# Optimization experiments

Hardware: AMD Instinct MI355X
Metric: run time of the kernel (lower is better)

Reference implementation:

```python
import jax, jax.numpy as jnp
import numpy as np

N = 20000        # nodes
E = 160000       # directed edges (before self loops)
NODE_DIM = 1287
HEADS = 4
C1, C2, C3 = 128, 256, 128
ACT_SLOPE = 0.15   # module's LeakyReLU between layers
GAT_SLOPE = 0.2    # PyG GATConv default negative_slope


def _gat_layer(x, src, dst, W, att_src, att_dst, bias, heads, out_dim, concat):
    # x: [N, in] ; W: [in, heads*out] ; att_*: [heads, out] ; bias: [heads*out] or [out]
    h = (x @ W).reshape(N, heads, out_dim)                      # [N, H, C]
    a_s = jnp.einsum('nhc,hc->nh', h, att_src)                  # [N, H]
    a_d = jnp.einsum('nhc,hc->nh', h, att_dst)                  # [N, H]
    e = jax.nn.leaky_relu(a_s[src] + a_d[dst], GAT_SLOPE)       # [Etot, H]
    # segment softmax over incoming edges of each dst node (self loops => no empty segments)
    m = jax.ops.segment_max(e, dst, num_segments=N)             # [N, H]
    w = jnp.exp(e - m[dst])
    den = jax.ops.segment_sum(w, dst, num_segments=N)           # [N, H]
    alpha = w / den[dst]                                        # [Etot, H]
    msg = h[src] * alpha[:, :, None]                            # [Etot, H, C]
    out = jax.ops.segment_sum(msg, dst, num_segments=N)         # [N, H, C]
    out = out.reshape(N, heads * out_dim) if concat else out.mean(axis=1)
    return out + bias


def setup_inputs() -> dict:
    key = jax.random.key(0)
    ks = jax.random.split(key, 22)
    s = 0.05
    x = jax.random.normal(ks[0], (N, NODE_DIM), jnp.float32)
    edge_index = jax.random.randint(ks[1], (2, E), 0, N, dtype=jnp.int64)
    inp = {
        'x': x, 'edge_index': edge_index,
        'W1': jax.random.normal(ks[2], (NODE_DIM, HEADS * C1), jnp.float32) * s,
        'as1': jax.random.normal(ks[3], (HEADS, C1), jnp.float32) * s,
        'ad1': jax.random.normal(ks[4], (HEADS, C1), jnp.float32) * s,
        'b1': jnp.zeros((HEADS * C1,), jnp.float32),
        'W2': jax.random.normal(ks[5], (HEADS * C1, HEADS * C2), jnp.float32) * s,
        'as2': jax.random.normal(ks[6], (HEADS, C2), jnp.float32) * s,
        'ad2': jax.random.normal(ks[7], (HEADS, C2), jnp.float32) * s,
        'b2': jnp.zeros((HEADS * C2,), jnp.float32),
        # conv3: 1024 -> 128, 1 head, no concat
        'W3': jax.random.normal(ks[8], (HEADS * C2, C3), jnp.float32) * s,
        'as3': jax.random.normal(ks[9], (1, C3), jnp.float32) * s,
        'ad3': jax.random.normal(ks[10], (1, C3), jnp.float32) * s,
        'b3': jnp.zeros((C3,), jnp.float32),
        # pre_fc: 128 -> 16
        'pw': jax.random.normal(ks[11], (C3, 16), jnp.float32) * s,
        'pb': jnp.zeros((16,), jnp.float32),
        # fc fallback: Linear(16,32) -> LeakyReLU(0.15) -> Linear(32,2)
        'f1w': jax.random.normal(ks[12], (16, 32), jnp.float32) * s,
        'f1b': jnp.zeros((32,), jnp.float32),
        'f2w': jax.random.normal(ks[13], (32, 2), jnp.float32) * s,
        'f2b': jnp.zeros((2,), jnp.float32),
    }
    return inp


def reference(x, edge_index, W1, as1, ad1, b1, W2, as2, ad2, b2,
              W3, as3, ad3, b3, pw, pb, f1w, f1b, f2w, f2b):
    loop = jnp.arange(N, dtype=edge_index.dtype)
    src = jnp.concatenate([edge_index[0], loop])   # PyG add_self_loops=True
    dst = jnp.concatenate([edge_index[1], loop])
    h = _gat_layer(x, src, dst, W1, as1, ad1, b1, HEADS, C1, True)
    h = jax.nn.leaky_relu(h, ACT_SLOPE)            # dropout = identity (eval)
    h = _gat_layer(h, src, dst, W2, as2, ad2, b2, HEADS, C2, True)
    h = jax.nn.leaky_relu(h, ACT_SLOPE)
    h = _gat_layer(h, src, dst, W3, as3, ad3, b3, 1, C3, False)
    h = jax.nn.leaky_relu(h, ACT_SLOPE)
    h = h @ pw + pb                                 # pre_fc (128 -> 16)
    h = jax.nn.leaky_relu(h @ f1w + f1b, ACT_SLOPE)
    return h @ f2w + f2b                            # [N, 2] logits
```

## Files before the change

kernel.cpp:

```cpp
#include <hip/hip_runtime.h>
#include <hip/hip_bf16.h>
#include <cstdint>
#include <cstddef>

#define LRELU(x, s) ((x) > 0.f ? (x) : (s) * (x))

typedef __attribute__((ext_vector_type(8))) short bf16x8;
typedef __attribute__((ext_vector_type(4))) float f32x4;

__device__ __forceinline__ float bflo(uint v) { return __uint_as_float(v << 16); }
__device__ __forceinline__ float bfhi(uint v) { return __uint_as_float(v & 0xffff0000u); }
__device__ __forceinline__ ushort f2bf(float f) {
  const uint u = __float_as_uint(f);
  return (ushort)((u + 0x7fffu + ((u >> 16) & 1u)) >> 16);
}

__device__ __forceinline__ void async16(const ushort* g, ushort* l) {
  __builtin_amdgcn_global_load_lds(
      (const __attribute__((address_space(1))) unsigned int*)g,
      (__attribute__((address_space(3))) unsigned int*)l, 16, 0, 0);
}

#define WAITCNT_VM(n) (0xF70 | (n))

__global__ void cast_pad_rows(const float* __restrict__ in, ushort* __restrict__ out,
                              int rows, int K, int Kp) {
  const int P4 = Kp >> 2;
  const long long idx = (long long)blockIdx.x * blockDim.x + threadIdx.x;
  if (idx >= (long long)rows * P4) return;
  const int r = (int)(idx / P4);
  const int c = ((int)(idx - (long long)r * P4)) << 2;
  const float* p = in + (size_t)r * K + c;
  float v0 = 0.f, v1 = 0.f, v2 = 0.f, v3 = 0.f;
  if (c + 3 < K) { v0 = p[0]; v1 = p[1]; v2 = p[2]; v3 = p[3]; }
  else {
    if (c + 0 < K) v0 = p[0];
    if (c + 1 < K) v1 = p[1];
    if (c + 2 < K) v2 = p[2];
    if (c + 3 < K) v3 = p[3];
  }
  uint2 o;
  o.x = (uint)f2bf(v0) | ((uint)f2bf(v1) << 16);
  o.y = (uint)f2bf(v2) | ((uint)f2bf(v3) << 16);
  *(uint2*)(out + (size_t)r * Kp + c) = o;
}

__global__ void cast_W_T(const float* __restrict__ W, ushort* __restrict__ Wt,
                         int K, int Nn, int Kp) {
  __shared__ float tile[32][33];
  const int kt = blockIdx.x * 32;
  const int nt = blockIdx.y * 32;
  const int tx = threadIdx.x;
  const int ty = threadIdx.y;
  for (int r = ty; r < 32; r += 8) {
    const int k = kt + r, nn = nt + tx;
    tile[r][tx] = (k < K && nn < Nn) ? W[(size_t)k * Nn + nn] : 0.f;
  }
  __syncthreads();
  for (int r = ty; r < 32; r += 8) {
    const int nn = nt + r, k = kt + tx;
    if (nn < Nn && k < Kp) Wt[(size_t)nn * Kp + k] = f2bf(tile[tx][r]);
  }
}

template <int TM>
__global__ __launch_bounds__(256) void gemm_bf16(
    const ushort* __restrict__ A, const ushort* __restrict__ Bt, ushort* __restrict__ C,
    int M, int N, int Kp,
    const float* __restrict__ AS, const float* __restrict__ AD,
    float* __restrict__ asb, float* __restrict__ adb, int H, int headC) {
  constexpr int MI = TM / 32;
  constexpr int LPG = (TM == 128) ? 4 : 3;
  __shared__ ushort sA[2 * TM * 32];
  __shared__ ushort sB[2 * 128 * 32];
  const int tid = threadIdx.x;
  const int wave = tid >> 6;
  const int lane = tid & 63;
  const int tilesN = N >> 7;
  const int bx = blockIdx.x % tilesN;
  const int by = blockIdx.x / tilesN;
  const int wrow = (wave >> 1) * (TM / 2);
  const int wcol = (wave & 1) * 64;
  const int quad = lane >> 4;
  const int ml = lane & 15;

  const int seg = (lane & 3) * 8;
  const int rB0 = wave * 32 + (lane >> 2);
  const int gB0 = bx * 128 + rB0;
  const ushort* pB0 = Bt + (size_t)gB0 * Kp + seg;
  const ushort* pB1 = Bt + (size_t)(gB0 + 16) * Kp + seg;
  ushort* lB0 = &sB[(wave * 32) * 32];
  ushort* lB1 = &sB[(wave * 32 + 16) * 32];
  const ushort *pA0, *pA1;
  ushort *lA0, *lA1;
  if constexpr (TM == 128) {
    const int r0 = wave * 32 + (lane >> 2);
    pA0 = A + (size_t)min(by * TM + r0, M - 1) * Kp + seg;
    pA1 = A + (size_t)min(by * TM + r0 + 16, M - 1) * Kp + seg;
    lA0 = &sA[(wave * 32) * 32];
    lA1 = &sA[(wave * 32 + 16) * 32];
  } else {
    const int r0 = wave * 16 + (lane >> 2);
    pA0 = A + (size_t)min(by * TM + r0, M - 1) * Kp + seg;
    pA1 = nullptr;
    lA0 = &sA[(wave * 16) * 32];
    lA1 = nullptr;
  }

  const int nIter = Kp >> 5;
  auto issue = [&](int it, int p) {
    const int k0 = it << 5;
    const int oa = p * TM * 32;
    const int ob_ = p * 128 * 32;
    async16(pA0 + k0, lA0 + oa);
    if constexpr (TM == 128) async16(pA1 + k0, lA1 + oa);
    async16(pB0 + k0, lB0 + ob_);
    async16(pB1 + k0, lB1 + ob_);
  };

  f32x4 acc[MI][4];
#pragma unroll
  for (int mi = 0; mi < MI; mi++)
#pragma unroll
    for (int ni = 0; ni < 4; ni++)
#pragma unroll
      for (int e = 0; e < 4; e++) acc[mi][ni][e] = 0.f;

  issue(0, 0);
  if (nIter > 1) issue(1, 1);
  int p = 0;
  for (int it = 0; it < nIter; ++it) {
    if (it + 1 < nIter) __builtin_amdgcn_s_waitcnt(WAITCNT_VM(LPG));
    else __builtin_amdgcn_s_waitcnt(WAITCNT_VM(0));
    __builtin_amdgcn_s_barrier();
    const ushort* bA = &sA[p * TM * 32];
    const ushort* bB = &sB[p * 128 * 32];
    bf16x8 af[MI], bfr[4];
#pragma unroll
    for (int mi = 0; mi < MI; mi++)
      af[mi] = *(const bf16x8*)&bA[(wrow + mi * 16 + ml) * 32 + quad * 8];
#pragma unroll
    for (int ni = 0; ni < 4; ni++)
      bfr[ni] = *(const bf16x8*)&bB[(wcol + ni * 16 + ml) * 32 + quad * 8];
#pragma unroll
    for (int mi = 0; mi < MI; mi++)
#pragma unroll
      for (int ni = 0; ni < 4; ni++)
        acc[mi][ni] = __builtin_amdgcn_mfma_f32_16x16x32_bf16(af[mi], bfr[ni], acc[mi][ni], 0, 0, 0);
    if (it + 2 < nIter) {
      __builtin_amdgcn_s_barrier();
      issue(it + 2, p);
    }
    p ^= 1;
  }

#pragma unroll
  for (int mi = 0; mi < MI; mi++) {
#pragma unroll
    for (int r = 0; r < 4; r++) {
      const int row = by * TM + wrow + mi * 16 + quad * 4 + r;
      if (row < M) {
#pragma unroll
        for (int ni = 0; ni < 4; ni++) {
          const int col = bx * 128 + wcol + ni * 16 + ml;
          C[(size_t)row * N + col] = f2bf(acc[mi][ni][r]);
        }
      }
    }
  }

  if (asb != nullptr) {
    float asv[4], adv[4];
#pragma unroll
    for (int ni = 0; ni < 4; ni++) {
      const int col = bx * 128 + wcol + ni * 16 + ml;
      asv[ni] = AS[col];
      adv[ni] = AD[col];
    }
    const int hh = (bx * 128 + wcol) / headC;
#pragma unroll
    for (int mi = 0; mi < MI; mi++) {
#pragma unroll
      for (int r = 0; r < 4; r++) {
        float ps = acc[mi][0][r] * asv[0] + acc[mi][1][r] * asv[1] +
                   acc[mi][2][r] * asv[2] + acc[mi][3][r] * asv[3];
        float pd = acc[mi][0][r] * adv[0] + acc[mi][1][r] * adv[1] +
                   acc[mi][2][r] * adv[2] + acc[mi][3][r] * adv[3];
#pragma unroll
        for (int off = 1; off < 16; off <<= 1) {
          ps += __shfl_xor(ps, off);
          pd += __shfl_xor(pd, off);
        }
        if (ml == 0) {
          const int row = by * TM + wrow + mi * 16 + quad * 4 + r;
          if (row < M) {
            atomicAdd(&asb[row * H + hh], ps);
            atomicAdd(&adb[row * H + hh], pd);
          }
        }
      }
    }
  }
}

__global__ void count_deg(const int* __restrict__ dst, int E, int* __restrict__ deg) {
  const int t = blockIdx.x * blockDim.x + threadIdx.x;
  if (t < E) atomicAdd(&deg[dst[t]], 1);
}

__global__ __launch_bounds__(1024) void scan_kernel(const int* __restrict__ deg,
                                                    int* __restrict__ rowptr,
                                                    int* __restrict__ cursor, int n) {
  __shared__ int swsum[16];
  __shared__ int carry_s;
  const int t = threadIdx.x;
  const int wv = t >> 6, lane = t & 63;
  if (t == 0) carry_s = 0;
  __syncthreads();
  for (int base = 0; base < n; base += 1024) {
    const int i = base + t;
    const int v = (i < n) ? (deg[i] + 1) : 0;
    int sc = v;
#pragma unroll
    for (int off = 1; off < 64; off <<= 1) {
      const int u = __shfl_up(sc, off);
      if (lane >= off) sc += u;
    }
    if (lane == 63) swsum[wv] = sc;
    __syncthreads();
    if (t < 16) {
      int x = swsum[t];
#pragma unroll
      for (int off = 1; off < 16; off <<= 1) {
        const int u = __shfl_up(x, off);
        if (t >= off) x += u;
      }
      swsum[t] = x;
    }
    __syncthreads();
    const int incl = sc + (wv == 0 ? 0 : swsum[wv - 1]) + carry_s;
    if (i < n) { rowptr[i + 1] = incl; cursor[i] = incl - v; }
    if (base == 0 && t == 0) rowptr[0] = 0;
    __syncthreads();
    if (t == 0) carry_s += swsum[15];
    __syncthreads();
  }
}

__global__ void scatter_edges(const int* __restrict__ esrc, const int* __restrict__ edst,
                              int E, int Etot, int* __restrict__ cursor,
                              int* __restrict__ csr_src) {
  const int t = blockIdx.x * blockDim.x + threadIdx.x;
  if (t >= Etot) return;
  int s, d;
  if (t < E) { s = esrc[t]; d = edst[t]; } else { s = t - E; d = s; }
  const int pos = atomicAdd(&cursor[d], 1);
  csr_src[pos] = s;
}

template <int H, int C>
__global__ __launch_bounds__(256) void gat_agg_wave(
    const ushort* __restrict__ hb, const int* __restrict__ rowptr,
    const int* __restrict__ csr_src, const float* __restrict__ a_s,
    const float* __restrict__ a_d, const float* __restrict__ bias,
    ushort* __restrict__ outb, float act_slope, int Nn) {
  constexpr int HC = H * C;
  constexpr int NU = HC / 2;
  constexpr int PPT = NU / 128;
  const int n = blockIdx.x * 4 + (threadIdx.x >> 6);
  const int lane = threadIdx.x & 63;
  if (n >= Nn) return;
  float ad_n[H];
#pragma unroll
  for (int h = 0; h < H; h++) ad_n[h] = a_d[n * H + h];
  const int start = rowptr[n], end = rowptr[n + 1];
  f32x4 acc[PPT];
#pragma unroll
  for (int q = 0; q < PPT; q++)
#pragma unroll
    for (int e = 0; e < 4; e++) acc[q][e] = 0.f;
  float den[H];
#pragma unroll
  for (int h = 0; h < H; h++) den[h] = 0.f;

  for (int base = start; base < end; base += 64) {
    const int cnt = min(64, end - base);
    int s = 0;
    float w[H];
#pragma unroll
    for (int h = 0; h < H; h++) w[h] = 0.f;
    if (lane < cnt) {
      s = csr_src[base + lane];
      float asv[H];
      if constexpr (H == 4) {
        const float4 t4 = *(const float4*)(a_s + s * 4);
        asv[0] = t4.x; asv[1] = t4.y; asv[2] = t4.z; asv[3] = t4.w;
      } else {
        asv[0] = a_s[s];
      }
#pragma unroll
      for (int h = 0; h < H; h++) {
        float lg = asv[h] + ad_n[h];
        lg = LRELU(lg, 0.2f);
        w[h] = __expf(lg);
        den[h] += w[h];
      }
    }
    for (int j = 0; j < cnt; j++) {
      const int sj = __shfl(s, j);
      float wj[H];
#pragma unroll
      for (int h = 0; h < H; h++) wj[h] = __shfl(w[h], j);
      const uint2* hp = (const uint2*)(hb + (size_t)sj * HC);
#pragma unroll
      for (int q = 0; q < PPT; q++) {
        const int pu = q * 128 + lane * 2;
        const uint2 v = hp[q * 64 + lane];
        const float wq = wj[(2 * pu) / C];
        acc[q][0] += wq * bflo(v.x);
        acc[q][1] += wq * bfhi(v.x);
        acc[q][2] += wq * bflo(v.y);
        acc[q][3] += wq * bfhi(v.y);
      }
    }
  }
#pragma unroll
  for (int h = 0; h < H; h++) {
#pragma unroll
    for (int off = 1; off < 64; off <<= 1) den[h] += __shfl_xor(den[h], off);
    den[h] = 1.f / den[h];
  }
#pragma unroll
  for (int q = 0; q < PPT; q++) {
    const int pu = q * 128 + lane * 2;
    const float iv = den[(2 * pu) / C];
    const float4 b4 = *(const float4*)(bias + 2 * pu);
    const float o0 = LRELU(acc[q][0] * iv + b4.x, act_slope);
    const float o1 = LRELU(acc[q][1] * iv + b4.y, act_slope);
    const float o2 = LRELU(acc[q][2] * iv + b4.z, act_slope);
    const float o3 = LRELU(acc[q][3] * iv + b4.w, act_slope);
    uint2 o;
    o.x = (uint)f2bf(o0) | ((uint)f2bf(o1) << 16);
    o.y = (uint)f2bf(o2) | ((uint)f2bf(o3) << 16);
    ((uint2*)outb)[(size_t)n * (NU / 2) + q * 64 + lane] = o;
  }
}

__global__ __launch_bounds__(64) void gat_agg3_mlp(
    const ushort* __restrict__ hb, const int* __restrict__ rowptr,
    const int* __restrict__ csr_src, const float* __restrict__ a_s,
    const float* __restrict__ a_d, const float* __restrict__ b3,
    const float* __restrict__ pw, const float* __restrict__ pb,
    const float* __restrict__ f1w, const float* __restrict__ f1b,
    const float* __restrict__ f2w, const float* __restrict__ f2b,
    float* __restrict__ out) {
  const int n = blockIdx.x;
  const int tid = threadIdx.x;
  __shared__ float sx[128];
  __shared__ float s1[16];
  __shared__ float s2[32];
  const float ad_n = a_d[n];
  const int start = rowptr[n], end = rowptr[n + 1];
  float2 acc = make_float2(0.f, 0.f);
  float den = 0.f;
  for (int base = start; base < end; base += 64) {
    const int cnt = min(64, end - base);
    int s = 0;
    float w = 0.f;
    if (tid < cnt) {
      s = csr_src[base + tid];
      float lg = a_s[s] + ad_n;
      lg = LRELU(lg, 0.2f);
      w = __expf(lg);
      den += w;
    }
    for (int j = 0; j < cnt; j++) {
      const int sj = __shfl(s, j);
      const float wj = __shfl(w, j);
      const uint v = ((const uint*)(hb + (size_t)sj * 128))[tid];
      acc.x += wj * bflo(v);
      acc.y += wj * bfhi(v);
    }
  }
#pragma unroll
  for (int off = 1; off < 64; off <<= 1) den += __shfl_xor(den, off);
  const float iv = 1.f / den;
  sx[2 * tid]     = LRELU(acc.x * iv + b3[2 * tid], 0.15f);
  sx[2 * tid + 1] = LRELU(acc.y * iv + b3[2 * tid + 1], 0.15f);
  __syncthreads();
  if (tid < 16) {
    float a = pb[tid];
    for (int c = 0; c < 128; c++) a += sx[c] * pw[c * 16 + tid];
    s1[tid] = a;
  }
  __syncthreads();
  if (tid < 32) {
    float a = f1b[tid];
    for (int c = 0; c < 16; c++) a += s1[c] * f1w[c * 32 + tid];
    s2[tid] = LRELU(a, 0.15f);
  }
  __syncthreads();
  if (tid < 2) {
    float a = f2b[tid];
    for (int c = 0; c < 32; c++) a += s2[c] * f2w[c * 2 + tid];
    out[(size_t)n * 2 + tid] = a;
  }
}

extern "C" void kernel_launch(void* const* d_in, const int* in_sizes, int n_in,
                              void* d_out, int out_size, void* d_ws, size_t ws_size,
                              hipStream_t stream) {
  const float* x   = (const float*)d_in[0];
  const int* ei    = (const int*)d_in[1];
  const float* W1  = (const float*)d_in[2];
  const float* as1 = (const float*)d_in[3];
  const float* ad1 = (const float*)d_in[4];
  const float* b1  = (const float*)d_in[5];
  const float* W2  = (const float*)d_in[6];
  const float* as2 = (const float*)d_in[7];
  const float* ad2 = (const float*)d_in[8];
  const float* b2  = (const float*)d_in[9];
  const float* W3  = (const float*)d_in[10];
  const float* as3 = (const float*)d_in[11];
  const float* ad3 = (const float*)d_in[12];
  const float* b3  = (const float*)d_in[13];
  const float* pw  = (const float*)d_in[14];
  const float* pb  = (const float*)d_in[15];
  const float* f1w = (const float*)d_in[16];
  const float* f1b = (const float*)d_in[17];
  const float* f2w = (const float*)d_in[18];
  const float* f2b = (const float*)d_in[19];
  float* out = (float*)d_out;

  const int N = in_sizes[0] / 1287;
  const int E = in_sizes[1] / 2;
  const int Etot = E + N;
  const int* esrc = ei;
  const int* edst = ei + E;
  const int K1 = 1287, K1p = 1312;

  char* ws = (char*)d_ws;
  size_t off = 0;
  auto alloc = [&](size_t bytes) -> void* {
    void* p = ws + off;
    off = (off + bytes + 255) & ~(size_t)255;
    return p;
  };
  ushort* hb  = (ushort*)alloc((size_t)N * 1024 * 2);
  ushort* ob  = (ushort*)alloc((size_t)N * 1024 * 2);
  ushort* xb  = (ushort*)alloc((size_t)N * K1p * 2);
  ushort* W1t = (ushort*)alloc((size_t)512 * K1p * 2);
  ushort* W2t = (ushort*)alloc((size_t)1024 * 512 * 2);
  ushort* W3t = (ushort*)alloc((size_t)128 * 1024 * 2);
  float* av   = (float*)alloc((size_t)N * 8 * sizeof(float));
  int* deg    = (int*)alloc((size_t)N * sizeof(int));
  int* rowptr = (int*)alloc((size_t)(N + 1) * sizeof(int));
  int* cursor = (int*)alloc((size_t)N * sizeof(int));
  int* csr    = (int*)alloc((size_t)Etot * sizeof(int));
  float* asb = av;
  float* adb = av + (size_t)N * 4;

  hipMemsetAsync(deg, 0, (size_t)N * sizeof(int), stream);
  count_deg<<<(E + 255) / 256, 256, 0, stream>>>(edst, E, deg);
  scan_kernel<<<1, 1024, 0, stream>>>(deg, rowptr, cursor, N);
  scatter_edges<<<(Etot + 255) / 256, 256, 0, stream>>>(esrc, edst, E, Etot, cursor, csr);

  {
    const long long nx = (long long)N * (K1p / 4);
    cast_pad_rows<<<(int)((nx + 255) / 256), 256, 0, stream>>>(x, xb, N, K1, K1p);
    cast_W_T<<<dim3(K1p / 32, (512 + 31) / 32), dim3(32, 8), 0, stream>>>(W1, W1t, K1, 512, K1p);
    cast_W_T<<<dim3(512 / 32, 1024 / 32), dim3(32, 8), 0, stream>>>(W2, W2t, 512, 1024, 512);
    cast_W_T<<<dim3(1024 / 32, 128 / 32), dim3(32, 8), 0, stream>>>(W3, W3t, 1024, 128, 1024);
  }

  const int tilesM = (N + 127) / 128;
  const int tilesM64 = (N + 63) / 64;
  const int aggBlocks = (N + 3) / 4;

  {
    const int H = 4, C = 128, HC = 512;
    hipMemsetAsync(av, 0, (size_t)N * 8 * sizeof(float), stream);
    gemm_bf16<128><<<tilesM * (HC / 128), 256, 0, stream>>>(xb, W1t, hb, N, HC, K1p,
                                                            as1, ad1, asb, adb, H, C);
    gat_agg_wave<4, 128><<<aggBlocks, 256, 0, stream>>>(hb, rowptr, csr, asb, adb,
                                                        b1, ob, 0.15f, N);
  }
  {
    const int H = 4, C = 256, HC = 1024;
    hipMemsetAsync(av, 0, (size_t)N * 8 * sizeof(float), stream);
    gemm_bf16<128><<<tilesM * (HC / 128), 256, 0, stream>>>(ob, W2t, hb, N, HC, 512,
                                                            as2, ad2, asb, adb, H, C);
    gat_agg_wave<4, 256><<<aggBlocks, 256, 0, stream>>>(hb, rowptr, csr, asb, adb,
                                                        b2, ob, 0.15f, N);
  }
  {
    const int HC = 128;
    hipMemsetAsync(av, 0, (size_t)N * 8 * sizeof(float), stream);
    gemm_bf16<64><<<tilesM64 * (HC / 128), 256, 0, stream>>>(ob, W3t, hb, N, HC, 1024,
                                                             as3, ad3, asb, adb, 1, 128);
    gat_agg3_mlp<<<N, 64, 0, stream>>>(hb, rowptr, csr, asb, adb, b3,
                                       pw, pb, f1w, f1b, f2w, f2b, out);
  }
}
```

Measured before the change: 525.6 us.

## Reorder layer-2 GAT to aggregate before projecting, fold attention into precomputed vectors

Layer 2 now computes attention logits directly from the 512-wide input using precomputed W2·att vectors. It then aggregates the 512-wide input features per head before the GEMM, with the GEMM reading head-specific slices of the aggregated buffer and applying bias plus LeakyReLU in its epilogue. This shrinks gather traffic from 1024-wide to 512-wide rows per edge, at the cost of writing a 2048-wide aggregated buffer. The GEMM also moves to a triple-buffered LDS pipeline that issues loads right after the barrier, dropping the second barrier, and uses M-major block ordering.

Result: slower. 549.3 us (+4.5%).

```diff
diff --git a/kernel.cpp b/kernel.cpp
--- a/kernel.cpp
+++ b/kernel.cpp
@@ -63,45 +63,61 @@
   }
 }
 
+__global__ void make_v2(const float* __restrict__ W2, const float* __restrict__ as2,
+                        const float* __restrict__ ad2, float* __restrict__ v) {
+  const int t = blockIdx.x * blockDim.x + threadIdx.x;
+  if (t >= 4096) return;
+  const int k = t >> 3, j = t & 7;
+  const int h = j & 3;
+  const float* att = (j >= 4) ? ad2 : as2;
+  const float* wrow = W2 + (size_t)k * 1024 + h * 256;
+  const float* ap = att + h * 256;
+  float a = 0.f;
+  for (int c = 0; c < 256; c++) a += wrow[c] * ap[c];
+  v[k * 8 + j] = a;
+}
+
 template <int TM>
 __global__ __launch_bounds__(256) void gemm_bf16(
     const ushort* __restrict__ A, const ushort* __restrict__ Bt, ushort* __restrict__ C,
-    int M, int N, int Kp,
+    int M, int N, int Kp, int Ars, int AheadStride, int headColsA,
+    const float* __restrict__ bias, float slope,
     const float* __restrict__ AS, const float* __restrict__ AD,
     float* __restrict__ asb, float* __restrict__ adb, int H, int headC) {
   constexpr int MI = TM / 32;
   constexpr int LPG = (TM == 128) ? 4 : 3;
-  __shared__ ushort sA[2 * TM * 32];
-  __shared__ ushort sB[2 * 128 * 32];
+  __shared__ ushort sA[3 * TM * 32];
+  __shared__ ushort sB[3 * 128 * 32];
   const int tid = threadIdx.x;
   const int wave = tid >> 6;
   const int lane = tid & 63;
-  const int tilesN = N >> 7;
-  const int bx = blockIdx.x % tilesN;
-  const int by = blockIdx.x / tilesN;
+  const int tilesM = (M + TM - 1) / TM;
+  const int by = blockIdx.x % tilesM;
+  const int bx = blockIdx.x / tilesM;
   const int wrow = (wave >> 1) * (TM / 2);
   const int wcol = (wave & 1) * 64;
   const int quad = lane >> 4;
   const int ml = lane & 15;
 
+  const int head = AheadStride ? (bx * 128) / headColsA : 0;
+  const size_t Aoff = (size_t)head * AheadStride;
   const int seg = (lane & 3) * 8;
   const int rB0 = wave * 32 + (lane >> 2);
-  const int gB0 = bx * 128 + rB0;
-  const ushort* pB0 = Bt + (size_t)gB0 * Kp + seg;
-  const ushort* pB1 = Bt + (size_t)(gB0 + 16) * Kp + seg;
+  const ushort* pB0 = Bt + (size_t)(bx * 128 + rB0) * Kp + seg;
+  const ushort* pB1 = Bt + (size_t)(bx * 128 + rB0 + 16) * Kp + seg;
   ushort* lB0 = &sB[(wave * 32) * 32];
   ushort* lB1 = &sB[(wave * 32 + 16) * 32];
   const ushort *pA0, *pA1;
   ushort *lA0, *lA1;
   if constexpr (TM == 128) {
     const int r0 = wave * 32 + (lane >> 2);
-    pA0 = A + (size_t)min(by * TM + r0, M - 1) * Kp + seg;
-    pA1 = A + (size_t)min(by * TM + r0 + 16, M - 1) * Kp + seg;
+    pA0 = A + (size_t)min(by * TM + r0, M - 1) * Ars + Aoff + seg;
+    pA1 = A + (size_t)min(by * TM + r0 + 16, M - 1) * Ars + Aoff + seg;
     lA0 = &sA[(wave * 32) * 32];
     lA1 = &sA[(wave * 32 + 16) * 32];
   } else {
     const int r0 = wave * 16 + (lane >> 2);
-    pA0 = A + (size_t)min(by * TM + r0, M - 1) * Kp + seg;
+    pA0 = A + (size_t)min(by * TM + r0, M - 1) * Ars + Aoff + seg;
     pA1 = nullptr;
     lA0 = &sA[(wave * 16) * 32];
     lA1 = nullptr;
@@ -133,6 +149,10 @@
     if (it + 1 < nIter) __builtin_amdgcn_s_waitcnt(WAITCNT_VM(LPG));
     else __builtin_amdgcn_s_waitcnt(WAITCNT_VM(0));
     __builtin_amdgcn_s_barrier();
+    if (it + 2 < nIter) {
+      const int pw = p ? p - 1 : 2;
+      issue(it + 2, pw);
+    }
     const ushort* bA = &sA[p * TM * 32];
     const ushort* bB = &sB[p * 128 * 32];
     bf16x8 af[MI], bfr[4];
@@ -147,11 +167,7 @@
 #pragma unroll
       for (int ni = 0; ni < 4; ni++)
         acc[mi][ni] = __builtin_amdgcn_mfma_f32_16x16x32_bf16(af[mi], bfr[ni], acc[mi][ni], 0, 0, 0);
-    if (it + 2 < nIter) {
-      __builtin_amdgcn_s_barrier();
-      issue(it + 2, p);
-    }
-    p ^= 1;
+    p = (p == 2) ? 0 : p + 1;
   }
 
 #pragma unroll
@@ -163,7 +179,9 @@
 #pragma unroll
         for (int ni = 0; ni < 4; ni++) {
           const int col = bx * 128 + wcol + ni * 16 + ml;
-          C[(size_t)row * N + col] = f2bf(acc[mi][ni][r]);
+          float v = acc[mi][ni][r];
+          if (bias) v = LRELU(v + bias[col], slope);
+          C[(size_t)row * N + col] = f2bf(v);
         }
       }
     }
@@ -343,6 +361,99 @@
     o.x = (uint)f2bf(o0) | ((uint)f2bf(o1) << 16);
     o.y = (uint)f2bf(o2) | ((uint)f2bf(o3) << 16);
     ((uint2*)outb)[(size_t)n * (NU / 2) + q * 64 + lane] = o;
+  }
+}
+
+__global__ __launch_bounds__(256) void att_dots_v(
+    const ushort* __restrict__ ob, const float* __restrict__ v,
+    float* __restrict__ asb, float* __restrict__ adb, int Nn) {
+  const int n = blockIdx.x * 4 + (threadIdx.x >> 6);
+  const int lane = threadIdx.x & 63;
+  if (n >= Nn) return;
+  const uint4 hv = ((const uint4*)(ob + (size_t)n * 512))[lane];
+  const float x[8] = {bflo(hv.x), bfhi(hv.x), bflo(hv.y), bfhi(hv.y),
+                      bflo(hv.z), bfhi(hv.z), bflo(hv.w), bfhi(hv.w)};
+  float a[8] = {0.f, 0.f, 0.f, 0.f, 0.f, 0.f, 0.f, 0.f};
+  const int k0 = lane * 8;
+#pragma unroll
+  for (int e = 0; e < 8; e++) {
+    const float4 v0 = *(const float4*)(v + (size_t)(k0 + e) * 8);
+    const float4 v1 = *(const float4*)(v + (size_t)(k0 + e) * 8 + 4);
+    a[0] += x[e] * v0.x; a[1] += x[e] * v0.y; a[2] += x[e] * v0.z; a[3] += x[e] * v0.w;
+    a[4] += x[e] * v1.x; a[5] += x[e] * v1.y; a[6] += x[e] * v1.z; a[7] += x[e] * v1.w;
+  }
+#pragma unroll
+  for (int off = 1; off < 64; off <<= 1)
+#pragma unroll
+    for (int j = 0; j < 8; j++) a[j] += __shfl_xor(a[j], off);
+  if (lane == 0) {
+    *(float4*)(asb + n * 4) = make_float4(a[0], a[1], a[2], a[3]);
+    *(float4*)(adb + n * 4) = make_float4(a[4], a[5], a[6], a[7]);
+  }
+}
+
+__global__ __launch_bounds__(256) void gat_agg_h4(
+    const ushort* __restrict__ ob, const int* __restrict__ rowptr,
+    const int* __restrict__ csr_src, const float* __restrict__ asb,
+    const float* __restrict__ adb, ushort* __restrict__ agg, int Nn) {
+  const int n = blockIdx.x * 4 + (threadIdx.x >> 6);
+  const int lane = threadIdx.x & 63;
+  if (n >= Nn) return;
+  const float4 adn = *(const float4*)(adb + n * 4);
+  const float ad_n[4] = {adn.x, adn.y, adn.z, adn.w};
+  const int start = rowptr[n], end = rowptr[n + 1];
+  float acc[4][8];
+#pragma unroll
+  for (int h = 0; h < 4; h++)
+#pragma unroll
+    for (int e = 0; e < 8; e++) acc[h][e] = 0.f;
+  float den[4] = {0.f, 0.f, 0.f, 0.f};
+
+  for (int base = start; base < end; base += 64) {
+    const int cnt = min(64, end - base);
+    int s = 0;
+    float w[4] = {0.f, 0.f, 0.f, 0.f};
+    if (lane < cnt) {
+      s = csr_src[base + lane];
+      const float4 t4 = *(const float4*)(asb + s * 4);
+      const float av4[4] = {t4.x, t4.y, t4.z, t4.w};
+#pragma unroll
+      for (int h = 0; h < 4; h++) {
+        float lg = av4[h] + ad_n[h];
+        lg = LRELU(lg, 0.2f);
+        w[h] = __expf(lg);
+        den[h] += w[h];
+      }
+    }
+    for (int j = 0; j < cnt; j++) {
+      const int sj = __shfl(s, j);
+      float wj[4];
+#pragma unroll
+      for (int h = 0; h < 4; h++) wj[h] = __shfl(w[h], j);
+      const uint4 hv = ((const uint4*)(ob + (size_t)sj * 512))[lane];
+      const float xx[8] = {bflo(hv.x), bfhi(hv.x), bflo(hv.y), bfhi(hv.y),
+                           bflo(hv.z), bfhi(hv.z), bflo(hv.w), bfhi(hv.w)};
+#pragma unroll
+      for (int h = 0; h < 4; h++)
+#pragma unroll
+        for (int e = 0; e < 8; e++) acc[h][e] += wj[h] * xx[e];
+    }
+  }
+#pragma unroll
+  for (int h = 0; h < 4; h++) {
+#pragma unroll
+    for (int off = 1; off < 64; off <<= 1) den[h] += __shfl_xor(den[h], off);
+    den[h] = 1.f / den[h];
+  }
+#pragma unroll
+  for (int h = 0; h < 4; h++) {
+    const float iv = den[h];
+    uint4 o;
+    o.x = (uint)f2bf(acc[h][0] * iv) | ((uint)f2bf(acc[h][1] * iv) << 16);
+    o.y = (uint)f2bf(acc[h][2] * iv) | ((uint)f2bf(acc[h][3] * iv) << 16);
+    o.z = (uint)f2bf(acc[h][4] * iv) | ((uint)f2bf(acc[h][5] * iv) << 16);
+    o.w = (uint)f2bf(acc[h][6] * iv) | ((uint)f2bf(acc[h][7] * iv) << 16);
+    ((uint4*)(agg + (size_t)n * 2048 + h * 512))[lane] = o;
   }
 }
 
@@ -446,17 +557,19 @@
     off = (off + bytes + 255) & ~(size_t)255;
     return p;
   };
-  ushort* hb  = (ushort*)alloc((size_t)N * 1024 * 2);
-  ushort* ob  = (ushort*)alloc((size_t)N * 1024 * 2);
-  ushort* xb  = (ushort*)alloc((size_t)N * K1p * 2);
-  ushort* W1t = (ushort*)alloc((size_t)512 * K1p * 2);
-  ushort* W2t = (ushort*)alloc((size_t)1024 * 512 * 2);
-  ushort* W3t = (ushort*)alloc((size_t)128 * 1024 * 2);
-  float* av   = (float*)alloc((size_t)N * 8 * sizeof(float));
-  int* deg    = (int*)alloc((size_t)N * sizeof(int));
-  int* rowptr = (int*)alloc((size_t)(N + 1) * sizeof(int));
-  int* cursor = (int*)alloc((size_t)N * sizeof(int));
-  int* csr    = (int*)alloc((size_t)Etot * sizeof(int));
+  ushort* hb   = (ushort*)alloc((size_t)N * 1024 * 2);
+  ushort* ob   = (ushort*)alloc((size_t)N * 512 * 2);
+  ushort* agg2 = (ushort*)alloc((size_t)N * 2048 * 2);
+  ushort* xb   = (ushort*)alloc((size_t)N * K1p * 2);
+  ushort* W1t  = (ushort*)alloc((size_t)512 * K1p * 2);
+  ushort* W2t  = (ushort*)alloc((size_t)1024 * 512 * 2);
+  ushort* W3t  = (ushort*)alloc((size_t)128 * 1024 * 2);
+  float* v2    = (float*)alloc((size_t)512 * 8 * sizeof(float));
+  float* av    = (float*)alloc((size_t)N * 8 * sizeof(float));
+  int* deg     = (int*)alloc((size_t)N * sizeof(int));
+  int* rowptr  = (int*)alloc((size_t)(N + 1) * sizeof(int));
+  int* cursor  = (int*)alloc((size_t)N * sizeof(int));
+  int* csr     = (int*)alloc((size_t)Etot * sizeof(int));
   float* asb = av;
   float* adb = av + (size_t)N * 4;
 
@@ -471,34 +584,27 @@
     cast_W_T<<<dim3(K1p / 32, (512 + 31) / 32), dim3(32, 8), 0, stream>>>(W1, W1t, K1, 512, K1p);
     cast_W_T<<<dim3(512 / 32, 1024 / 32), dim3(32, 8), 0, stream>>>(W2, W2t, 512, 1024, 512);
     cast_W_T<<<dim3(1024 / 32, 128 / 32), dim3(32, 8), 0, stream>>>(W3, W3t, 1024, 128, 1024);
+    make_v2<<<16, 256, 0, stream>>>(W2, as2, ad2, v2);
   }
 
   const int tilesM = (N + 127) / 128;
   const int tilesM64 = (N + 63) / 64;
-  const int aggBlocks = (N + 3) / 4;
-
-  {
-    const int H = 4, C = 128, HC = 512;
-    hipMemsetAsync(av, 0, (size_t)N * 8 * sizeof(float), stream);
-    gemm_bf16<128><<<tilesM * (HC / 128), 256, 0, stream>>>(xb, W1t, hb, N, HC, K1p,
-                                                            as1, ad1, asb, adb, H, C);
-    gat_agg_wave<4, 128><<<aggBlocks, 256, 0, stream>>>(hb, rowptr, csr, asb, adb,
-                                                        b1, ob, 0.15f, N);
-  }
-  {
-    const int H = 4, C = 256, HC = 1024;
-    hipMemsetAsync(av, 0, (size_t)N * 8 * sizeof(float), stream);
-    gemm_bf16<128><<<tilesM * (HC / 128), 256, 0, stream>>>(ob, W2t, hb, N, HC, 512,
-                                                            as2, ad2, asb, adb, H, C);
-    gat_agg_wave<4, 256><<<aggBlocks, 256, 0, stream>>>(hb, rowptr, csr, asb, adb,
-                                                        b2, ob, 0.15f, N);
-  }
-  {
-    const int HC = 128;
-    hipMemsetAsync(av, 0, (size_t)N * 8 * sizeof(float), stream);
-    gemm_bf16<64><<<tilesM64 * (HC / 128), 256, 0, stream>>>(ob, W3t, hb, N, HC, 1024,
-                                                             as3, ad3, asb, adb, 1, 128);
-    gat_agg3_mlp<<<N, 64, 0, stream>>>(hb, rowptr, csr, asb, adb, b3,
-                                       pw, pb, f1w, f1b, f2w, f2b, out);
-  }
-}
+  const int nodeBlocks = (N + 3) / 4;
+
+  hipMemsetAsync(av, 0, (size_t)N * 8 * sizeof(float), stream);
+  gemm_bf16<128><<<tilesM * 4, 256, 0, stream>>>(xb, W1t, hb, N, 512, K1p, K1p, 0, 1,
+                                                 nullptr, 0.f, as1, ad1, asb, adb, 4, 128);
+  gat_agg_wave<4, 128><<<nodeBlocks, 256, 0, stream>>>(hb, rowptr, csr, asb, adb,
+                                                       b1, ob, 0.15f, N);
+
+  att_dots_v<<<nodeBlocks, 256, 0, stream>>>(ob, v2, asb, adb, N);
+  gat_agg_h4<<<nodeBlocks, 256, 0, stream>>>(ob, rowptr, csr, asb, adb, agg2, N);
+  gemm_bf16<128><<<tilesM * 8, 256, 0, stream>>>(agg2, W2t, hb, N, 1024, 512, 2048, 512, 256,
+                                                 b2, 0.15f, nullptr, nullptr, nullptr, nullptr, 0, 0);
+
+  hipMemsetAsync(av, 0, (size_t)N * 8 * sizeof(float), stream);
+  gemm_bf16<64><<<tilesM64, 256, 0, stream>>>(hb, W3t, ob, N, 128, 1024, 1024, 0, 1,
+                                              nullptr, 0.f, as3, ad3, asb, adb, 1, 128);
+  gat_agg3_mlp<<<N, 64, 0, stream>>>(ob, rowptr, csr, asb, adb, b3,
+                                     pw, pb, f1w, f1b, f2w, f2b, out);
+}
```

## Triple-buffer GEMM LDS pipeline and widen aggregation loads to 16 bytes

Applied to the files above, without the earlier changes.

The GEMM moves from two LDS stages to three. The prefetch for iteration it+2 is now issued right after the barrier, before the MFMAs, and the second barrier per K-step is gone. This is meant to overlap global-to-LDS loads with compute and cut synchronisation, at the cost of 1.5x shared memory per block, which may lower occupancy. The aggregation kernel reads each gathered neighbour row as uint4 (8 bf16 per lane) instead of uint2, halving load instructions, though each lane now holds twice as many accumulators. A separate A-row-stride parameter is added, and the host launches are flattened without changing behaviour.

Result: no change. 527.6 us (+0.4%).

```diff
diff --git a/kernel.cpp b/kernel.cpp
--- a/kernel.cpp
+++ b/kernel.cpp
@@ -66,13 +66,13 @@
 template <int TM>
 __global__ __launch_bounds__(256) void gemm_bf16(
     const ushort* __restrict__ A, const ushort* __restrict__ Bt, ushort* __restrict__ C,
-    int M, int N, int Kp,
+    int M, int N, int Kp, int Ars,
     const float* __restrict__ AS, const float* __restrict__ AD,
     float* __restrict__ asb, float* __restrict__ adb, int H, int headC) {
   constexpr int MI = TM / 32;
   constexpr int LPG = (TM == 128) ? 4 : 3;
-  __shared__ ushort sA[2 * TM * 32];
-  __shared__ ushort sB[2 * 128 * 32];
+  __shared__ ushort sA[3 * TM * 32];
+  __shared__ ushort sB[3 * 128 * 32];
   const int tid = threadIdx.x;
   const int wave = tid >> 6;
   const int lane = tid & 63;
@@ -86,22 +86,21 @@
 
   const int seg = (lane & 3) * 8;
   const int rB0 = wave * 32 + (lane >> 2);
-  const int gB0 = bx * 128 + rB0;
-  const ushort* pB0 = Bt + (size_t)gB0 * Kp + seg;
-  const ushort* pB1 = Bt + (size_t)(gB0 + 16) * Kp + seg;
+  const ushort* pB0 = Bt + (size_t)(bx * 128 + rB0) * Kp + seg;
+  const ushort* pB1 = Bt + (size_t)(bx * 128 + rB0 + 16) * Kp + seg;
   ushort* lB0 = &sB[(wave * 32) * 32];
   ushort* lB1 = &sB[(wave * 32 + 16) * 32];
   const ushort *pA0, *pA1;
   ushort *lA0, *lA1;
   if constexpr (TM == 128) {
     const int r0 = wave * 32 + (lane >> 2);
-    pA0 = A + (size_t)min(by * TM + r0, M - 1) * Kp + seg;
-    pA1 = A + (size_t)min(by * TM + r0 + 16, M - 1) * Kp + seg;
+    pA0 = A + (size_t)min(by * TM + r0, M - 1) * Ars + seg;
+    pA1 = A + (size_t)min(by * TM + r0 + 16, M - 1) * Ars + seg;
     lA0 = &sA[(wave * 32) * 32];
     lA1 = &sA[(wave * 32 + 16) * 32];
   } else {
     const int r0 = wave * 16 + (lane >> 2);
-    pA0 = A + (size_t)min(by * TM + r0, M - 1) * Kp + seg;
+    pA0 = A + (size_t)min(by * TM + r0, M - 1) * Ars + seg;
     pA1 = nullptr;
     lA0 = &sA[(wave * 16) * 32];
     lA1 = nullptr;
@@ -133,6 +132,10 @@
     if (it + 1 < nIter) __builtin_amdgcn_s_waitcnt(WAITCNT_VM(LPG));
     else __builtin_amdgcn_s_waitcnt(WAITCNT_VM(0));
     __builtin_amdgcn_s_barrier();
+    if (it + 2 < nIter) {
+      const int pw = p ? p - 1 : 2;
+      issue(it + 2, pw);
+    }
     const ushort* bA = &sA[p * TM * 32];
     const ushort* bB = &sB[p * 128 * 32];
     bf16x8 af[MI], bfr[4];
@@ -147,11 +150,7 @@
 #pragma unroll
       for (int ni = 0; ni < 4; ni++)
         acc[mi][ni] = __builtin_amdgcn_mfma_f32_16x16x32_bf16(af[mi], bfr[ni], acc[mi][ni], 0, 0, 0);
-    if (it + 2 < nIter) {
-      __builtin_amdgcn_s_barrier();
-      issue(it + 2, p);
-    }
-    p ^= 1;
+    p = (p == 2) ? 0 : p + 1;
   }
 
 #pragma unroll
@@ -265,8 +264,8 @@
     const float* __restrict__ a_d, const float* __restrict__ bias,
     ushort* __restrict__ outb, float act_slope, int Nn) {
   constexpr int HC = H * C;
-  constexpr int NU = HC / 2;
-  constexpr int PPT = NU / 128;
+  constexpr int NQ = HC / 8;
+  constexpr int PPT = NQ / 64;
   const int n = blockIdx.x * 4 + (threadIdx.x >> 6);
   const int lane = threadIdx.x & 63;
   if (n >= Nn) return;
@@ -274,11 +273,11 @@
 #pragma unroll
   for (int h = 0; h < H; h++) ad_n[h] = a_d[n * H + h];
   const int start = rowptr[n], end = rowptr[n + 1];
-  f32x4 acc[PPT];
+  float acc[PPT][8];
 #pragma unroll
   for (int q = 0; q < PPT; q++)
 #pragma unroll
-    for (int e = 0; e < 4; e++) acc[q][e] = 0.f;
+    for (int e = 0; e < 8; e++) acc[q][e] = 0.f;
   float den[H];
 #pragma unroll
   for (int h = 0; h < H; h++) den[h] = 0.f;
@@ -311,16 +310,20 @@
       float wj[H];
 #pragma unroll
       for (int h = 0; h < H; h++) wj[h] = __shfl(w[h], j);
-      const uint2* hp = (const uint2*)(hb + (size_t)sj * HC);
+      const uint4* hp = (const uint4*)(hb + (size_t)sj * HC);
 #pragma unroll
       for (int q = 0; q < PPT; q++) {
-        const int pu = q * 128 + lane * 2;
-        const uint2 v = hp[q * 64 + lane];
-        const float wq = wj[(2 * pu) / C];
+        const int iq = q * 64 + lane;
+        const uint4 v = hp[iq];
+        const float wq = wj[(8 * iq) / C];
         acc[q][0] += wq * bflo(v.x);
         acc[q][1] += wq * bfhi(v.x);
         acc[q][2] += wq * bflo(v.y);
         acc[q][3] += wq * bfhi(v.y);
+        acc[q][4] += wq * bflo(v.z);
+        acc[q][5] += wq * bfhi(v.z);
+        acc[q][6] += wq * bflo(v.w);
+        acc[q][7] += wq * bfhi(v.w);
       }
     }
   }
@@ -332,17 +335,18 @@
   }
 #pragma unroll
   for (int q = 0; q < PPT; q++) {
-    const int pu = q * 128 + lane * 2;
-    const float iv = den[(2 * pu) / C];
-    const float4 b4 = *(const float4*)(bias + 2 * pu);
-    const float o0 = LRELU(acc[q][0] * iv + b4.x, act_slope);
-    const float o1 = LRELU(acc[q][1] * iv + b4.y, act_slope);
-    const float o2 = LRELU(acc[q][2] * iv + b4.z, act_slope);
-    const float o3 = LRELU(acc[q][3] * iv + b4.w, act_slope);
-    uint2 o;
-    o.x = (uint)f2bf(o0) | ((uint)f2bf(o1) << 16);
-    o.y = (uint)f2bf(o2) | ((uint)f2bf(o3) << 16);
-    ((uint2*)outb)[(size_t)n * (NU / 2) + q * 64 + lane] = o;
+    const int iq = q * 64 + lane;
+    const int c0 = 8 * iq;
+    const float iv = den[c0 / C];
+    uint4 o;
+    float vv[8];
+#pragma unroll
+    for (int e = 0; e < 8; e++) vv[e] = LRELU(acc[q][e] * iv + bias[c0 + e], act_slope);
+    o.x = (uint)f2bf(vv[0]) | ((uint)f2bf(vv[1]) << 16);
+    o.y = (uint)f2bf(vv[2]) | ((uint)f2bf(vv[3]) << 16);
+    o.z = (uint)f2bf(vv[4]) | ((uint)f2bf(vv[5]) << 16);
+    o.w = (uint)f2bf(vv[6]) | ((uint)f2bf(vv[7]) << 16);
+    ((uint4*)outb)[(size_t)n * NQ + iq] = o;
   }
 }
 
@@ -475,30 +479,23 @@
 
   const int tilesM = (N + 127) / 128;
   const int tilesM64 = (N + 63) / 64;
-  const int aggBlocks = (N + 3) / 4;
-
-  {
-    const int H = 4, C = 128, HC = 512;
-    hipMemsetAsync(av, 0, (size_t)N * 8 * sizeof(float), stream);
-    gemm_bf16<128><<<tilesM * (HC / 128), 256, 0, stream>>>(xb, W1t, hb, N, HC, K1p,
-                                                            as1, ad1, asb, adb, H, C);
-    gat_agg_wave<4, 128><<<aggBlocks, 256, 0, stream>>>(hb, rowptr, csr, asb, adb,
-                                                        b1, ob, 0.15f, N);
-  }
-  {
-    const int H = 4, C = 256, HC = 1024;
-    hipMemsetAsync(av, 0, (size_t)N * 8 * sizeof(float), stream);
-    gemm_bf16<128><<<tilesM * (HC / 128), 256, 0, stream>>>(ob, W2t, hb, N, HC, 512,
-                                                            as2, ad2, asb, adb, H, C);
-    gat_agg_wave<4, 256><<<aggBlocks, 256, 0, stream>>>(hb, rowptr, csr, asb, adb,
-                                                        b2, ob, 0.15f, N);
-  }
-  {
-    const int HC = 128;
-    hipMemsetAsync(av, 0, (size_t)N * 8 * sizeof(float), stream);
-    gemm_bf16<64><<<tilesM64 * (HC / 128), 256, 0, stream>>>(ob, W3t, hb, N, HC, 1024,
-                                                             as3, ad3, asb, adb, 1, 128);
-    gat_agg3_mlp<<<N, 64, 0, stream>>>(hb, rowptr, csr, asb, adb, b3,
-                                       pw, pb, f1w, f1b, f2w, f2b, out);
-  }
-}
+  const int nodeBlocks = (N + 3) / 4;
+
+  hipMemsetAsync(av, 0, (size_t)N * 8 * sizeof(float), stream);
+  gemm_bf16<128><<<tilesM * 4, 256, 0, stream>>>(xb, W1t, hb, N, 512, K1p, K1p,
+                                                 as1, ad1, asb, adb, 4, 128);
+  gat_agg_wave<4, 128><<<nodeBlocks, 256, 0, stream>>>(hb, rowptr, csr, asb, adb,
+                                                       b1, ob, 0.15f, N);
+
+  hipMemsetAsync(av, 0, (size_t)N * 8 * sizeof(float), stream);
+  gemm_bf16<128><<<tilesM * 8, 256, 0, stream>>>(ob, W2t, hb, N, 1024, 512, 512,
+                                                 as2, ad2, asb, adb, 4, 256);
+  gat_agg_wave<4, 256><<<nodeBlocks, 256, 0, stream>>>(hb, rowptr, csr, asb, adb,
+                                                       b2, ob, 0.15f, N);
+
+  hipMemsetAsync(av, 0, (size_t)N * 8 * sizeof(float), stream);
+  gemm_bf16<64><<<tilesM64, 256, 0, stream>>>(ob, W3t, hb, N, 128, 1024, 1024,
+                                              as3, ad3, asb, adb, 1, 128);
+  gat_agg3_mlp<<<N, 64, 0, stream>>>(hb, rowptr, csr, asb, adb, b3,
+                                     pw, pb, f1w, f1b, f2w, f2b, out);
+}
```
